# Performance work log

Measured on AMD Instinct MI355X. Metric: run time of the kernel, lower is better.

## Reference

```python
import jax, jax.numpy as jnp
import numpy as np

LN_EPS = 1e-5


def setup_inputs() -> dict:
    key = jax.random.key(0)
    ks = jax.random.split(key, 12)
    B, T, U, H, V = 4, 512, 128, 512, 41
    src = jax.random.normal(ks[0], (B, T, H), dtype=jnp.float32)
    tgt = jax.random.normal(ks[1], (B, U, H), dtype=jnp.float32)
    src_len = jax.random.randint(ks[2], (B,), 1, T + 1, dtype=jnp.int32)
    tgt_len = jax.random.randint(ks[3], (B,), 1, U + 1, dtype=jnp.int32)
    s = 1.0 / np.sqrt(H)
    W1 = jax.random.uniform(ks[4], (H, H), jnp.float32, -s, s)
    b1 = jax.random.uniform(ks[5], (H,), jnp.float32, -s, s)
    W2 = jax.random.uniform(ks[6], (H, H), jnp.float32, -s, s)
    b2 = jax.random.uniform(ks[7], (H,), jnp.float32, -s, s)
    ln_g = jnp.ones((H,), jnp.float32)
    ln_b = jnp.zeros((H,), jnp.float32)
    Wl = jax.random.uniform(ks[8], (H, V), jnp.float32, -s, s)
    bl = jax.random.uniform(ks[9], (V,), jnp.float32, -s, s)
    return dict(source_encodings=src, source_lengths=src_len,
                target_encodings=tgt, target_lengths=tgt_len,
                W1=W1, b1=b1, W2=W2, b2=b2, ln_g=ln_g, ln_b=ln_b,
                Wl=Wl, bl=bl)


def _f_target(tgt, W1, b1, W2, b2, ln_g, ln_b):
    h = jax.nn.gelu(tgt @ W1 + b1, approximate=False)  # exact GELU (torch default)
    h = h @ W2 + b2
    mu = jnp.mean(h, axis=-1, keepdims=True)
    var = jnp.var(h, axis=-1, keepdims=True)
    return (h - mu) * jax.lax.rsqrt(var + LN_EPS) * ln_g + ln_b


def reference(source_encodings, source_lengths, target_encodings, target_lengths,
              W1, b1, W2, b2, ln_g, ln_b, Wl, bl):
    tgt = _f_target(target_encodings, W1, b1, W2, b2, ln_g, ln_b)  # [B,U,H]
    # joint broadcast add: [B,T,1,H] + [B,1,U,H] -> [B,T,U,H]
    joint = source_encodings[:, :, None, :] + tgt[:, None, :, :]
    act = jnp.tanh(joint)
    out = act @ Wl + bl  # [B,T,U,V]
    return out, source_lengths, target_lengths
```

## Files before the change

kernel.cpp:

```cpp
#include <hip/hip_runtime.h>
#include <math.h>

#define Bb 4
#define Tt 512
#define Uu 128
#define Hh 512
#define Vv 41

typedef __attribute__((ext_vector_type(8))) short short8;
typedef __attribute__((ext_vector_type(4))) float f32x4;
typedef __attribute__((ext_vector_type(2))) float v2f;

__device__ __forceinline__ unsigned pack_bf16_rne(float hi, float lo) {
    unsigned xh = __float_as_uint(hi); xh += 0x7fffu + ((xh >> 16) & 1u);
    unsigned xl = __float_as_uint(lo); xl += 0x7fffu + ((xl >> 16) & 1u);
    return __builtin_amdgcn_perm(xh, xl, 0x07060302);
}

__device__ __forceinline__ unsigned short bf16_rne(float v) {
    unsigned x = __float_as_uint(v);
    x += 0x7fffu + ((x >> 16) & 1u);
    return (unsigned short)(x >> 16);
}

__device__ __forceinline__ float bf16lo(unsigned u) { return __uint_as_float(u << 16); }
__device__ __forceinline__ float bf16hi(unsigned u) { return __uint_as_float(u & 0xffff0000u); }

__device__ __forceinline__ float tanh_acc(float x) {
    float e = __expf(2.0f * x);
    return 1.0f - 2.0f * __builtin_amdgcn_rcpf(e + 1.0f);
}

__device__ __forceinline__ unsigned mob2(unsigned aw, float ts0, float ts1) {
    v2f tt = {bf16lo(aw), bf16hi(aw)};
    v2f ts = {ts0, ts1};
    v2f nm = ts + tt;
    v2f dn = ts * tt + (v2f){1.f, 1.f};
    v2f g;
    g.x = nm.x * __builtin_amdgcn_rcpf(dn.x);
    g.y = nm.y * __builtin_amdgcn_rcpf(dn.y);
    return __builtin_amdgcn_perm(__float_as_uint(g.y), __float_as_uint(g.x), 0x07060302);
}

__global__ __launch_bounds__(256) void prep_pack(
    const float* __restrict__ W1, const float* __restrict__ W2,
    const float* __restrict__ Wl, const float* __restrict__ tgt,
    unsigned short* __restrict__ Wp1, unsigned short* __restrict__ Wp2,
    unsigned short* __restrict__ Wpl3, unsigned short* __restrict__ tgtA,
    const int* __restrict__ sl, const int* __restrict__ tl,
    float* __restrict__ lenDst)
{
    __shared__ __align__(16) char smem[16640];
    const int bid = blockIdx.x, tid = threadIdx.x;

    if (bid >= 136) {
        unsigned short (*At)[520] = (unsigned short (*)[520])smem;
        const int rt = bid - 136;
        const float4* t4 = (const float4*)(tgt + (size_t)rt * 16 * Hh);
        #pragma unroll
        for (int j = 0; j < 8; ++j) {
            int fi = j * 256 + tid;
            int row = fi >> 7, c4 = fi & 127;
            float4 v = t4[fi];
            uint2 pk;
            pk.x = pack_bf16_rne(v.y, v.x);
            pk.y = pack_bf16_rne(v.w, v.z);
            *(uint2*)&At[row][c4 * 4] = pk;
        }
        __syncthreads();
        #pragma unroll
        for (int i = 0; i < 4; ++i) {
            int chunk = i * 256 + tid;
            int ks = chunk >> 6, l = chunk & 63;
            int q = l >> 4, nc = l & 15;
            short8 v = *(const short8*)&At[nc][ks * 32 + q * 8];
            *(short8*)(tgtA + ((size_t)(rt * 16 + ks) * 64 + l) * 8) = v;
        }
        return;
    }

    if (bid == 135 && tid < 2 * Bb)
        lenDst[tid] = (tid < Bb) ? (float)sl[tid] : (float)tl[tid - Bb];

    float (*T)[65] = (float (*)[65])smem;
    const float* Wsrc; unsigned short* Wdst; int k0, n0, isWl;
    if (bid < 64)       { Wsrc = W1; Wdst = Wp1; k0 = (bid >> 3) * 64; n0 = (bid & 7) * 64; isWl = 0; }
    else if (bid < 128) { Wsrc = W2; Wdst = Wp2; k0 = ((bid - 64) >> 3) * 64; n0 = ((bid - 64) & 7) * 64; isWl = 0; }
    else                { Wsrc = Wl; Wdst = Wpl3; k0 = (bid - 128) * 64; n0 = 0; isWl = 1; }

    #pragma unroll
    for (int i = 0; i < 16; ++i) {
        int idx = i * 256 + tid;
        int kk = idx >> 6, nn = idx & 63;
        float v;
        if (isWl) v = (nn < Vv) ? Wl[(k0 + kk) * Vv + nn] : 0.0f;
        else      v = Wsrc[(size_t)(k0 + kk) * 512 + n0 + nn];
        T[kk][nn] = v;
    }
    __syncthreads();

    #pragma unroll
    for (int i = 0; i < 2; ++i) {
        int task = i * 256 + tid;
        int nn = task & 63, kg = task >> 6;
        if (isWl && nn >= 48) continue;
        int n = n0 + nn, k = k0 + kg * 8;
        float e[8];
        #pragma unroll
        for (int j = 0; j < 8; ++j) e[j] = T[kg * 8 + j][nn];
        uint4 pk;
        pk.x = pack_bf16_rne(e[1], e[0]);
        pk.y = pack_bf16_rne(e[3], e[2]);
        pk.z = pack_bf16_rne(e[5], e[4]);
        pk.w = pack_bf16_rne(e[7], e[6]);
        int ntg = n >> 4, ncol = n & 15;
        int ks = (k >> 5) & 15, quad = (k >> 3) & 3;
        int lane = quad * 16 + ncol;
        size_t slot = isWl ? (size_t)((ks * 3 + ntg) * 64 + lane)
                           : (size_t)((ntg * 16 + ks) * 64 + lane);
        *(uint4*)(Wdst + slot * 8) = pk;
    }
}

__global__ __launch_bounds__(128) void gemm_t1(
    const unsigned short* __restrict__ tgtA,
    const unsigned short* __restrict__ Wp1, const float* __restrict__ b1,
    unsigned short* __restrict__ h1A)
{
    __shared__ unsigned short At[16][72];
    const int nb = blockIdx.x, rt = blockIdx.y;
    const int tid = threadIdx.x, lane = tid & 63, w = tid >> 6;
    const int ncol = lane & 15, quad = lane >> 4;
    const int nt0 = nb * 4 + w * 2;

    const unsigned short* ap = tgtA + ((size_t)rt * 1024 + lane) * 8;
    const unsigned short* bp = Wp1 + (size_t)lane * 8;

    f32x4 acc0 = (f32x4){0.f,0.f,0.f,0.f}, acc1 = (f32x4){0.f,0.f,0.f,0.f};
    short8 ac  = *(const short8*)(ap);
    short8 b0c = *(const short8*)(bp + (size_t)nt0 * 8192);
    short8 b1c = *(const short8*)(bp + (size_t)(nt0 + 1) * 8192);

    #pragma unroll
    for (int ks = 0; ks < 16; ++ks) {
        short8 an, b0n, b1n;
        if (ks < 15) {
            an  = *(const short8*)(ap + (ks + 1) * 512);
            b0n = *(const short8*)(bp + (size_t)nt0 * 8192 + (ks + 1) * 512);
            b1n = *(const short8*)(bp + (size_t)(nt0 + 1) * 8192 + (ks + 1) * 512);
        }
        acc0 = __builtin_amdgcn_mfma_f32_16x16x32_bf16(ac, b0c, acc0, 0, 0, 0);
        acc1 = __builtin_amdgcn_mfma_f32_16x16x32_bf16(ac, b1c, acc1, 0, 0, 0);
        ac = an; b0c = b0n; b1c = b1n;
    }

    #pragma unroll
    for (int nt = 0; nt < 2; ++nt) {
        int n = nb * 64 + w * 32 + nt * 16 + ncol;
        float bias = b1[n];
        f32x4 A = nt ? acc1 : acc0;
        #pragma unroll
        for (int r = 0; r < 4; ++r) {
            float v = A[r] + bias;
            float g = 0.5f * v * (1.0f + erff(v * 0.70710678118654752f));
            At[quad * 4 + r][w * 32 + nt * 16 + ncol] = bf16_rne(g);
        }
    }
    __syncthreads();

    {
        int l = lane;
        short8 v = *(const short8*)&At[l & 15][w * 32 + (l >> 4) * 8];
        int ksg = nb * 2 + w;
        *(short8*)(h1A + ((size_t)(rt * 16 + ksg) * 64 + l) * 8) = v;
    }
}

__global__ __launch_bounds__(512) void gemm_t2ln(
    const unsigned short* __restrict__ h1A,
    const unsigned short* __restrict__ Wp2, const float* __restrict__ b2,
    const float* __restrict__ ln_g, const float* __restrict__ ln_b,
    unsigned short* __restrict__ tgtPb)
{
    __shared__ float Ct[16][520];
    const int rt = blockIdx.x;
    const int tid = threadIdx.x, lane = tid & 63, w = tid >> 6;
    const int ncol = lane & 15, quad = lane >> 4;
    const int nt0 = w * 4;

    const unsigned short* ap = h1A + ((size_t)rt * 1024 + lane) * 8;
    const unsigned short* bp = Wp2 + (size_t)lane * 8 + (size_t)nt0 * 8192;

    f32x4 acc[4];
    #pragma unroll
    for (int i = 0; i < 4; ++i) acc[i] = (f32x4){0.f, 0.f, 0.f, 0.f};

    short8 ac = *(const short8*)(ap);
    short8 bc[4];
    #pragma unroll
    for (int i = 0; i < 4; ++i) bc[i] = *(const short8*)(bp + (size_t)i * 8192);

    #pragma unroll
    for (int ks = 0; ks < 16; ++ks) {
        short8 an, bn[4];
        if (ks < 15) {
            an = *(const short8*)(ap + (ks + 1) * 512);
            #pragma unroll
            for (int i = 0; i < 4; ++i)
                bn[i] = *(const short8*)(bp + (size_t)i * 8192 + (ks + 1) * 512);
        }
        #pragma unroll
        for (int i = 0; i < 4; ++i)
            acc[i] = __builtin_amdgcn_mfma_f32_16x16x32_bf16(ac, bc[i], acc[i], 0, 0, 0);
        ac = an;
        #pragma unroll
        for (int i = 0; i < 4; ++i) bc[i] = bn[i];
    }

    #pragma unroll
    for (int nt = 0; nt < 4; ++nt) {
        int n = w * 64 + nt * 16 + ncol;
        float bias = b2[n];
        #pragma unroll
        for (int r = 0; r < 4; ++r)
            Ct[quad * 4 + r][n] = acc[nt][r] + bias;
    }
    __syncthreads();

    #pragma unroll
    for (int rr = 0; rr < 2; ++rr) {
        const int row = w * 2 + rr;
        const float4* cr = (const float4*)&Ct[row][0];
        float4 v0 = cr[lane], v1 = cr[lane + 64];
        float s = v0.x + v0.y + v0.z + v0.w + v1.x + v1.y + v1.z + v1.w;
        float q = v0.x*v0.x + v0.y*v0.y + v0.z*v0.z + v0.w*v0.w
                + v1.x*v1.x + v1.y*v1.y + v1.z*v1.z + v1.w*v1.w;
        #pragma unroll
        for (int off = 32; off > 0; off >>= 1) {
            s += __shfl_xor(s, off, 64);
            q += __shfl_xor(q, off, 64);
        }
        float mu = s * (1.0f / Hh);
        float rs = rsqrtf(q * (1.0f / Hh) - mu * mu + 1e-5f);

        const int r = rt * 16 + row;
        const int bb = r >> 7, u = r & 127;
        #pragma unroll
        for (int j = 0; j < 2; ++j) {
            int k0 = j * 256 + lane * 4;
            float4 v = j ? v1 : v0;
            float4 g4 = ((const float4*)ln_g)[j * 64 + lane];
            float4 b4 = ((const float4*)ln_b)[j * 64 + lane];
            float4 o;
            o.x = tanh_acc((v.x - mu) * rs * g4.x + b4.x);
            o.y = tanh_acc((v.y - mu) * rs * g4.y + b4.y);
            o.z = tanh_acc((v.z - mu) * rs * g4.z + b4.z);
            o.w = tanh_acc((v.w - mu) * rs * g4.w + b4.w);
            uint2 pk;
            pk.x = pack_bf16_rne(o.y, o.x);
            pk.y = pack_bf16_rne(o.w, o.z);
            int chunk = k0 >> 3, half = (k0 >> 2) & 1;
            *(uint2*)(tgtPb + ((size_t)(bb * 64 + chunk) * 128 + u) * 8 + half * 4) = pk;
        }
    }
}

__global__ __launch_bounds__(256) void joint_mfma(
    const float* __restrict__ src, const unsigned short* __restrict__ tgtPb,
    const unsigned short* __restrict__ Wpl3, const float* __restrict__ bl,
    float* __restrict__ out)
{
    __shared__ float srcl[2 * Hh];
    __shared__ __align__(16) float tileC[2 * 64 * Vv];

    const int t0 = blockIdx.x * 2, b = blockIdx.y, uh = blockIdx.z;
    const int tid = threadIdx.x;
    const int lane = tid & 63, wave = tid >> 6;
    const int ncol = lane & 15, quad = lane >> 4;

    {
        const float4* s4 = (const float4*)(src + ((size_t)(b * Tt + t0)) * Hh);
        float4 v = s4[tid];
        v.x = tanh_acc(v.x); v.y = tanh_acc(v.y);
        v.z = tanh_acc(v.z); v.w = tanh_acc(v.w);
        ((float4*)srcl)[tid] = v;
    }

    const int u0 = uh * 64 + (wave & 1) * 32 + ncol;
    const unsigned short* apl = tgtPb + (size_t)b * 65536 + ((size_t)quad * 128 + u0) * 8;
    const unsigned short* bpl = Wpl3 + (size_t)lane * 8;

    uint4 Aa[2], Ac[2];
    short8 Bq[2][3];
    Aa[0] = *(const uint4*)(apl);
    Ac[0] = *(const uint4*)(apl + 128);
    Bq[0][0] = *(const short8*)(bpl);
    Bq[0][1] = *(const short8*)(bpl + 512);
    Bq[0][2] = *(const short8*)(bpl + 1024);
    apl += 4096; bpl += 1536;
    Aa[1] = *(const uint4*)(apl);
    Ac[1] = *(const uint4*)(apl + 128);
    Bq[1][0] = *(const short8*)(bpl);
    Bq[1][1] = *(const short8*)(bpl + 512);
    Bq[1][2] = *(const short8*)(bpl + 1024);
    apl += 4096; bpl += 1536;

    f32x4 acc[2][3];
    #pragma unroll
    for (int nt = 0; nt < 3; ++nt) {
        int n = nt * 16 + ncol;
        float bv = (n < Vv) ? bl[n] : 0.0f;
        acc[0][nt] = (f32x4){bv, bv, bv, bv};
        acc[1][nt] = (f32x4){bv, bv, bv, bv};
    }

    __syncthreads();
    const float* srow = srcl + (wave >> 1) * Hh;
    float4 sA = *(const float4*)(srow + quad * 8);
    float4 sB = *(const float4*)(srow + quad * 8 + 4);

    #pragma unroll
    for (int ks = 0; ks < 16; ++ks) {
        const int st = ks & 1;
        uint4 a = Aa[st], c = Ac[st];
        short8 B0 = Bq[st][0], B1 = Bq[st][1], B2 = Bq[st][2];

        if (ks + 2 < 16) {
            Aa[st] = *(const uint4*)(apl);
            Ac[st] = *(const uint4*)(apl + 128);
            Bq[st][0] = *(const short8*)(bpl);
            Bq[st][1] = *(const short8*)(bpl + 512);
            Bq[st][2] = *(const short8*)(bpl + 1024);
            apl += 4096; bpl += 1536;
        }
        float4 nsA, nsB;
        if (ks < 15) {
            nsA = *(const float4*)(srow + (ks + 1) * 32 + quad * 8);
            nsB = *(const float4*)(srow + (ks + 1) * 32 + quad * 8 + 4);
        }

        union { uint4 u; short8 s; } f0, f1;
        f0.u.x = mob2(a.x, sA.x, sA.y);
        f0.u.y = mob2(a.y, sA.z, sA.w);
        f0.u.z = mob2(a.z, sB.x, sB.y);
        f0.u.w = mob2(a.w, sB.z, sB.w);
        f1.u.x = mob2(c.x, sA.x, sA.y);
        f1.u.y = mob2(c.y, sA.z, sA.w);
        f1.u.z = mob2(c.z, sB.x, sB.y);
        f1.u.w = mob2(c.w, sB.z, sB.w);

        acc[0][0] = __builtin_amdgcn_mfma_f32_16x16x32_bf16(f0.s, B0, acc[0][0], 0, 0, 0);
        acc[1][0] = __builtin_amdgcn_mfma_f32_16x16x32_bf16(f1.s, B0, acc[1][0], 0, 0, 0);
        acc[0][1] = __builtin_amdgcn_mfma_f32_16x16x32_bf16(f0.s, B1, acc[0][1], 0, 0, 0);
        acc[1][1] = __builtin_amdgcn_mfma_f32_16x16x32_bf16(f1.s, B1, acc[1][1], 0, 0, 0);
        acc[0][2] = __builtin_amdgcn_mfma_f32_16x16x32_bf16(f0.s, B2, acc[0][2], 0, 0, 0);
        acc[1][2] = __builtin_amdgcn_mfma_f32_16x16x32_bf16(f1.s, B2, acc[1][2], 0, 0, 0);

        sA = nsA; sB = nsB;
    }

    {
        const int tloc = wave >> 1;
        const int ubr = (wave & 1) * 32;
        float* tc = tileC + tloc * (64 * Vv);
        #pragma unroll
        for (int mi = 0; mi < 2; ++mi) {
            #pragma unroll
            for (int nt = 0; nt < 3; ++nt) {
                int n = nt * 16 + ncol;
                if (n < Vv) {
                    #pragma unroll
                    for (int r = 0; r < 4; ++r)
                        tc[(ubr + mi * 16 + quad * 4 + r) * Vv + n] = acc[mi][nt][r];
                }
            }
        }
    }
    __syncthreads();
    {
        float* ob0 = out + (((size_t)(b * Tt + t0)) * Uu + uh * 64) * Vv;
        float* ob1 = out + (((size_t)(b * Tt + t0 + 1)) * Uu + uh * 64) * Vv;
        const float4* tc4 = (const float4*)tileC;
        #pragma unroll
        for (int i = 0; i < 3; ++i) {
            int idx = i * 256 + tid;
            if (idx < 656) {
                ((float4*)ob0)[idx] = tc4[idx];
                ((float4*)ob1)[idx] = tc4[656 + idx];
            }
        }
    }
}

extern "C" void kernel_launch(void* const* d_in, const int* in_sizes, int n_in,
                              void* d_out, int out_size, void* d_ws, size_t ws_size,
                              hipStream_t stream)
{
    const float* src  = (const float*)d_in[0];
    const int*   slen = (const int*)  d_in[1];
    const float* tgt  = (const float*)d_in[2];
    const int*   tlen = (const int*)  d_in[3];
    const float* W1   = (const float*)d_in[4];
    const float* b1   = (const float*)d_in[5];
    const float* W2   = (const float*)d_in[6];
    const float* b2   = (const float*)d_in[7];
    const float* ln_g = (const float*)d_in[8];
    const float* ln_b = (const float*)d_in[9];
    const float* Wl   = (const float*)d_in[10];
    const float* bl   = (const float*)d_in[11];

    float* out = (float*)d_out;
    char* ws = (char*)d_ws;
    unsigned short* tgtPb = (unsigned short*)(ws);
    unsigned short* Wp1   = (unsigned short*)(ws + 524288);
    unsigned short* Wp2   = (unsigned short*)(ws + 1048576);
    unsigned short* Wpl3  = (unsigned short*)(ws + 1572864);
    unsigned short* tgtA  = (unsigned short*)(ws + 1638400);
    unsigned short* h1A   = (unsigned short*)(ws + 2162688);

    hipLaunchKernelGGL(prep_pack, dim3(168), dim3(256), 0, stream,
                       W1, W2, Wl, tgt, Wp1, Wp2, Wpl3, tgtA,
                       slen, tlen, out + (size_t)Bb * Tt * Uu * Vv);
    hipLaunchKernelGGL(gemm_t1, dim3(8, 32), dim3(128), 0, stream,
                       tgtA, Wp1, b1, h1A);
    hipLaunchKernelGGL(gemm_t2ln, dim3(32), dim3(512), 0, stream,
                       h1A, Wp2, b2, ln_g, ln_b, tgtPb);
    hipLaunchKernelGGL(joint_mfma, dim3(Tt / 2, Bb, 2), dim3(256), 0, stream,
                       src, tgtPb, Wpl3, bl, out);
}
```

Baseline: 138.3 us.

## Fuse both target MLP GEMMs into one kernel and remap joint waves

Merges gemm_t1 (GEMM+GELU) and gemm_t2ln (GEMM+LayerNorm) into a single 32-block kernel that keeps the GELU output in shared memory, removing one launch and the h1A global round trip. This cuts the first GEMM's grid from 256 blocks to 32, so it runs with less parallelism. The joint kernel also changes its wave mapping: each wave now covers 16 u-rows for both t rows instead of 32 u-rows for one t. One A fragment load is then shared across both time steps, in place of two A loads per wave.

```diff
diff --git a/kernel.cpp b/kernel.cpp
--- a/kernel.cpp
+++ b/kernel.cpp
@@ -122,99 +122,84 @@
     }
 }
 
-__global__ __launch_bounds__(128) void gemm_t1(
+__global__ __launch_bounds__(512) void target_fused(
     const unsigned short* __restrict__ tgtA,
     const unsigned short* __restrict__ Wp1, const float* __restrict__ b1,
-    unsigned short* __restrict__ h1A)
-{
-    __shared__ unsigned short At[16][72];
-    const int nb = blockIdx.x, rt = blockIdx.y;
-    const int tid = threadIdx.x, lane = tid & 63, w = tid >> 6;
-    const int ncol = lane & 15, quad = lane >> 4;
-    const int nt0 = nb * 4 + w * 2;
-
-    const unsigned short* ap = tgtA + ((size_t)rt * 1024 + lane) * 8;
-    const unsigned short* bp = Wp1 + (size_t)lane * 8;
-
-    f32x4 acc0 = (f32x4){0.f,0.f,0.f,0.f}, acc1 = (f32x4){0.f,0.f,0.f,0.f};
-    short8 ac  = *(const short8*)(ap);
-    short8 b0c = *(const short8*)(bp + (size_t)nt0 * 8192);
-    short8 b1c = *(const short8*)(bp + (size_t)(nt0 + 1) * 8192);
-
-    #pragma unroll
-    for (int ks = 0; ks < 16; ++ks) {
-        short8 an, b0n, b1n;
-        if (ks < 15) {
-            an  = *(const short8*)(ap + (ks + 1) * 512);
-            b0n = *(const short8*)(bp + (size_t)nt0 * 8192 + (ks + 1) * 512);
-            b1n = *(const short8*)(bp + (size_t)(nt0 + 1) * 8192 + (ks + 1) * 512);
-        }
-        acc0 = __builtin_amdgcn_mfma_f32_16x16x32_bf16(ac, b0c, acc0, 0, 0, 0);
-        acc1 = __builtin_amdgcn_mfma_f32_16x16x32_bf16(ac, b1c, acc1, 0, 0, 0);
-        ac = an; b0c = b0n; b1c = b1n;
-    }
-
-    #pragma unroll
-    for (int nt = 0; nt < 2; ++nt) {
-        int n = nb * 64 + w * 32 + nt * 16 + ncol;
-        float bias = b1[n];
-        f32x4 A = nt ? acc1 : acc0;
-        #pragma unroll
-        for (int r = 0; r < 4; ++r) {
-            float v = A[r] + bias;
-            float g = 0.5f * v * (1.0f + erff(v * 0.70710678118654752f));
-            At[quad * 4 + r][w * 32 + nt * 16 + ncol] = bf16_rne(g);
-        }
-    }
-    __syncthreads();
-
-    {
-        int l = lane;
-        short8 v = *(const short8*)&At[l & 15][w * 32 + (l >> 4) * 8];
-        int ksg = nb * 2 + w;
-        *(short8*)(h1A + ((size_t)(rt * 16 + ksg) * 64 + l) * 8) = v;
-    }
-}
-
-__global__ __launch_bounds__(512) void gemm_t2ln(
-    const unsigned short* __restrict__ h1A,
     const unsigned short* __restrict__ Wp2, const float* __restrict__ b2,
     const float* __restrict__ ln_g, const float* __restrict__ ln_b,
     unsigned short* __restrict__ tgtPb)
 {
+    __shared__ unsigned short At[16][520];
     __shared__ float Ct[16][520];
+
     const int rt = blockIdx.x;
     const int tid = threadIdx.x, lane = tid & 63, w = tid >> 6;
     const int ncol = lane & 15, quad = lane >> 4;
-    const int nt0 = w * 4;
-
-    const unsigned short* ap = h1A + ((size_t)rt * 1024 + lane) * 8;
-    const unsigned short* bp = Wp2 + (size_t)lane * 8 + (size_t)nt0 * 8192;
+
+    const unsigned short* ap = tgtA + ((size_t)rt * 1024 + lane) * 8;
+    const unsigned short* bp1 = Wp1 + (size_t)lane * 8 + (size_t)(w * 4) * 8192;
+    const unsigned short* bp2 = Wp2 + (size_t)lane * 8 + (size_t)(w * 4) * 8192;
 
     f32x4 acc[4];
     #pragma unroll
     for (int i = 0; i < 4; ++i) acc[i] = (f32x4){0.f, 0.f, 0.f, 0.f};
 
-    short8 ac = *(const short8*)(ap);
-    short8 bc[4];
-    #pragma unroll
-    for (int i = 0; i < 4; ++i) bc[i] = *(const short8*)(bp + (size_t)i * 8192);
-
-    #pragma unroll
-    for (int ks = 0; ks < 16; ++ks) {
-        short8 an, bn[4];
-        if (ks < 15) {
-            an = *(const short8*)(ap + (ks + 1) * 512);
+    {
+        short8 ac = *(const short8*)(ap);
+        short8 bc[4];
+        #pragma unroll
+        for (int i = 0; i < 4; ++i) bc[i] = *(const short8*)(bp1 + (size_t)i * 8192);
+        #pragma unroll
+        for (int ks = 0; ks < 16; ++ks) {
+            short8 an, bn[4];
+            if (ks < 15) {
+                an = *(const short8*)(ap + (ks + 1) * 512);
+                #pragma unroll
+                for (int i = 0; i < 4; ++i)
+                    bn[i] = *(const short8*)(bp1 + (size_t)i * 8192 + (ks + 1) * 512);
+            }
             #pragma unroll
             for (int i = 0; i < 4; ++i)
-                bn[i] = *(const short8*)(bp + (size_t)i * 8192 + (ks + 1) * 512);
-        }
-        #pragma unroll
-        for (int i = 0; i < 4; ++i)
-            acc[i] = __builtin_amdgcn_mfma_f32_16x16x32_bf16(ac, bc[i], acc[i], 0, 0, 0);
-        ac = an;
-        #pragma unroll
-        for (int i = 0; i < 4; ++i) bc[i] = bn[i];
+                acc[i] = __builtin_amdgcn_mfma_f32_16x16x32_bf16(ac, bc[i], acc[i], 0, 0, 0);
+            ac = an;
+            #pragma unroll
+            for (int i = 0; i < 4; ++i) bc[i] = bn[i];
+        }
+    }
+
+    #pragma unroll
+    for (int nt = 0; nt < 4; ++nt) {
+        int n = w * 64 + nt * 16 + ncol;
+        float bias = b1[n];
+        #pragma unroll
+        for (int r = 0; r < 4; ++r) {
+            float v = acc[nt][r] + bias;
+            float g = 0.5f * v * (1.0f + erff(v * 0.70710678118654752f));
+            At[quad * 4 + r][n] = bf16_rne(g);
+        }
+        acc[nt] = (f32x4){0.f, 0.f, 0.f, 0.f};
+    }
+    __syncthreads();
+
+    {
+        short8 bc[4];
+        #pragma unroll
+        for (int i = 0; i < 4; ++i) bc[i] = *(const short8*)(bp2 + (size_t)i * 8192);
+        #pragma unroll
+        for (int ks = 0; ks < 16; ++ks) {
+            short8 bn[4];
+            if (ks < 15) {
+                #pragma unroll
+                for (int i = 0; i < 4; ++i)
+                    bn[i] = *(const short8*)(bp2 + (size_t)i * 8192 + (ks + 1) * 512);
+            }
+            short8 af = *(const short8*)&At[ncol][ks * 32 + quad * 8];
+            #pragma unroll
+            for (int i = 0; i < 4; ++i)
+                acc[i] = __builtin_amdgcn_mfma_f32_16x16x32_bf16(af, bc[i], acc[i], 0, 0, 0);
+            #pragma unroll
+            for (int i = 0; i < 4; ++i) bc[i] = bn[i];
+        }
     }
 
     #pragma unroll
@@ -286,20 +271,18 @@
         ((float4*)srcl)[tid] = v;
     }
 
-    const int u0 = uh * 64 + (wave & 1) * 32 + ncol;
+    const int u0 = uh * 64 + wave * 16 + ncol;
     const unsigned short* apl = tgtPb + (size_t)b * 65536 + ((size_t)quad * 128 + u0) * 8;
     const unsigned short* bpl = Wpl3 + (size_t)lane * 8;
 
-    uint4 Aa[2], Ac[2];
+    uint4 Aq[2];
     short8 Bq[2][3];
-    Aa[0] = *(const uint4*)(apl);
-    Ac[0] = *(const uint4*)(apl + 128);
+    Aq[0] = *(const uint4*)(apl);
     Bq[0][0] = *(const short8*)(bpl);
     Bq[0][1] = *(const short8*)(bpl + 512);
     Bq[0][2] = *(const short8*)(bpl + 1024);
     apl += 4096; bpl += 1536;
-    Aa[1] = *(const uint4*)(apl);
-    Ac[1] = *(const uint4*)(apl + 128);
+    Aq[1] = *(const uint4*)(apl);
     Bq[1][0] = *(const short8*)(bpl);
     Bq[1][1] = *(const short8*)(bpl + 512);
     Bq[1][2] = *(const short8*)(bpl + 1024);
@@ -315,39 +298,44 @@
     }
 
     __syncthreads();
-    const float* srow = srcl + (wave >> 1) * Hh;
-    float4 sA = *(const float4*)(srow + quad * 8);
-    float4 sB = *(const float4*)(srow + quad * 8 + 4);
+    const float* sr0 = srcl;
+    const float* sr1 = srcl + Hh;
+    float4 sA0 = *(const float4*)(sr0 + quad * 8);
+    float4 sB0 = *(const float4*)(sr0 + quad * 8 + 4);
+    float4 sA1 = *(const float4*)(sr1 + quad * 8);
+    float4 sB1 = *(const float4*)(sr1 + quad * 8 + 4);
 
     #pragma unroll
     for (int ks = 0; ks < 16; ++ks) {
         const int st = ks & 1;
-        uint4 a = Aa[st], c = Ac[st];
+        uint4 a = Aq[st];
         short8 B0 = Bq[st][0], B1 = Bq[st][1], B2 = Bq[st][2];
 
         if (ks + 2 < 16) {
-            Aa[st] = *(const uint4*)(apl);
-            Ac[st] = *(const uint4*)(apl + 128);
+            Aq[st] = *(const uint4*)(apl);
             Bq[st][0] = *(const short8*)(bpl);
             Bq[st][1] = *(const short8*)(bpl + 512);
             Bq[st][2] = *(const short8*)(bpl + 1024);
             apl += 4096; bpl += 1536;
         }
-        float4 nsA, nsB;
+        float4 nsA0, nsB0, nsA1, nsB1;
         if (ks < 15) {
-            nsA = *(const float4*)(srow + (ks + 1) * 32 + quad * 8);
-            nsB = *(const float4*)(srow + (ks + 1) * 32 + quad * 8 + 4);
+            const int o = (ks + 1) * 32 + quad * 8;
+            nsA0 = *(const float4*)(sr0 + o);
+            nsB0 = *(const float4*)(sr0 + o + 4);
+            nsA1 = *(const float4*)(sr1 + o);
+            nsB1 = *(const float4*)(sr1 + o + 4);
         }
 
         union { uint4 u; short8 s; } f0, f1;
-        f0.u.x = mob2(a.x, sA.x, sA.y);
-        f0.u.y = mob2(a.y, sA.z, sA.w);
-        f0.u.z = mob2(a.z, sB.x, sB.y);
-        f0.u.w = mob2(a.w, sB.z, sB.w);
-        f1.u.x = mob2(c.x, sA.x, sA.y);
-        f1.u.y = mob2(c.y, sA.z, sA.w);
-        f1.u.z = mob2(c.z, sB.x, sB.y);
-        f1.u.w = mob2(c.w, sB.z, sB.w);
+        f0.u.x = mob2(a.x, sA0.x, sA0.y);
+        f0.u.y = mob2(a.y, sA0.z, sA0.w);
+        f0.u.z = mob2(a.z, sB0.x, sB0.y);
+        f0.u.w = mob2(a.w, sB0.z, sB0.w);
+        f1.u.x = mob2(a.x, sA1.x, sA1.y);
+        f1.u.y = mob2(a.y, sA1.z, sA1.w);
+        f1.u.z = mob2(a.z, sB1.x, sB1.y);
+        f1.u.w = mob2(a.w, sB1.z, sB1.w);
 
         acc[0][0] = __builtin_amdgcn_mfma_f32_16x16x32_bf16(f0.s, B0, acc[0][0], 0, 0, 0);
         acc[1][0] = __builtin_amdgcn_mfma_f32_16x16x32_bf16(f1.s, B0, acc[1][0], 0, 0, 0);
@@ -356,23 +344,19 @@
         acc[0][2] = __builtin_amdgcn_mfma_f32_16x16x32_bf16(f0.s, B2, acc[0][2], 0, 0, 0);
         acc[1][2] = __builtin_amdgcn_mfma_f32_16x16x32_bf16(f1.s, B2, acc[1][2], 0, 0, 0);
 
-        sA = nsA; sB = nsB;
-    }
-
-    {
-        const int tloc = wave >> 1;
-        const int ubr = (wave & 1) * 32;
-        float* tc = tileC + tloc * (64 * Vv);
-        #pragma unroll
-        for (int mi = 0; mi < 2; ++mi) {
-            #pragma unroll
-            for (int nt = 0; nt < 3; ++nt) {
-                int n = nt * 16 + ncol;
-                if (n < Vv) {
-                    #pragma unroll
-                    for (int r = 0; r < 4; ++r)
-                        tc[(ubr + mi * 16 + quad * 4 + r) * Vv + n] = acc[mi][nt][r];
-                }
+        sA0 = nsA0; sB0 = nsB0; sA1 = nsA1; sB1 = nsB1;
+    }
+
+    #pragma unroll
+    for (int t = 0; t < 2; ++t) {
+        float* tc = tileC + t * (64 * Vv);
+        #pragma unroll
+        for (int nt = 0; nt < 3; ++nt) {
+            int n = nt * 16 + ncol;
+            if (n < Vv) {
+                #pragma unroll
+                for (int r = 0; r < 4; ++r)
+                    tc[(wave * 16 + quad * 4 + r) * Vv + n] = acc[t][nt][r];
             }
         }
     }
@@ -416,15 +400,12 @@
     unsigned short* Wp2   = (unsigned short*)(ws + 1048576);
     unsigned short* Wpl3  = (unsigned short*)(ws + 1572864);
     unsigned short* tgtA  = (unsigned short*)(ws + 1638400);
-    unsigned short* h1A   = (unsigned short*)(ws + 2162688);
 
     hipLaunchKernelGGL(prep_pack, dim3(168), dim3(256), 0, stream,
                        W1, W2, Wl, tgt, Wp1, Wp2, Wpl3, tgtA,
                        slen, tlen, out + (size_t)Bb * Tt * Uu * Vv);
-    hipLaunchKernelGGL(gemm_t1, dim3(8, 32), dim3(128), 0, stream,
-                       tgtA, Wp1, b1, h1A);
-    hipLaunchKernelGGL(gemm_t2ln, dim3(32), dim3(512), 0, stream,
-                       h1A, Wp2, b2, ln_g, ln_b, tgtPb);
+    hipLaunchKernelGGL(target_fused, dim3(32), dim3(512), 0, stream,
+                       tgtA, Wp1, b1, Wp2, b2, ln_g, ln_b, tgtPb);
     hipLaunchKernelGGL(joint_mfma, dim3(Tt / 2, Bb, 2), dim3(256), 0, stream,
                        src, tgtPb, Wpl3, bl, out);
 }
```

After: 135.1 us. -2.3%, faster.
